# Performance work log

Hardware: AMD Instinct MI355X
Metric: run time of the kernel (lower is better)

The kernel has to match this reference:

```python
import jax, jax.numpy as jnp
import numpy as np

TOPK = 2


def _conv2d(x, w, b):
    # x: (B, Cin, H, W), w: (Cout, Cin, 3, 3), SAME padding (padding=1)
    y = jax.lax.conv_general_dilated(
        x, w, window_strides=(1, 1), padding='SAME',
        dimension_numbers=('NCHW', 'OIHW', 'NCHW'))
    return y + b[None, :, None, None]


def _msunit(x2d, c1w, c1b, c2w, c2b):
    # TimesNet-style 2D unit: conv(1->d_model) -> GELU -> conv(d_model->1)
    h = jax.nn.gelu(_conv2d(x2d, c1w, c1b))
    return _conv2d(h, c2w, c2b)


def setup_inputs():
    B, T, H, DM = 256, 2048, 720, 64
    key = jax.random.key(0)
    ks = jax.random.split(key, 5)
    x = jax.random.normal(ks[0], (B, 1, T), jnp.float32)
    conv1_w = jax.random.normal(ks[1], (DM, 1, 3, 3), jnp.float32) * 0.1
    conv1_b = jnp.zeros((DM,), jnp.float32)
    conv2_w = jax.random.normal(ks[2], (1, DM, 3, 3), jnp.float32) * 0.1
    conv2_b = jnp.zeros((1,), jnp.float32)
    head_w = jax.random.normal(ks[3], (H, T), jnp.float32) * 0.02
    head_b = jnp.zeros((H,), jnp.float32)
    return {'x': x, 'conv1_w': conv1_w, 'conv1_b': conv1_b,
            'conv2_w': conv2_w, 'conv2_b': conv2_b,
            'head_w': head_w, 'head_b': head_b}


def reference(x, conv1_w, conv1_b, conv2_w, conv2_b, head_w, head_b):
    B, _, T = x.shape
    # FFT amplitude spectrum, batch-averaged, drop DC bin
    amp = jnp.abs(jnp.fft.rfft(x[:, 0, :], axis=-1)).mean(0)[1:]
    vals, idx = jax.lax.top_k(amp, TOPK)
    # data-dependent period selection (mirrors .item() calls in torch -> Python ints)
    freqs = np.asarray(idx) + 1
    P_list = [max(1, int(round(T / int(f)))) for f in freqs]
    weights = jax.nn.softmax(vals.astype(x.dtype))
    y = jnp.zeros_like(x)
    for i, P in enumerate(P_list):
        cols = (T + P - 1) // P
        pad = P * cols - T
        xp = jnp.pad(x, ((0, 0), (0, 0), (0, pad)))
        x2d = xp.reshape(B, 1, cols, P).transpose(0, 1, 3, 2)  # (B,1,P,cols)
        y2d = _msunit(x2d, conv1_w, conv1_b, conv2_w, conv2_b)  # (B,1,P,cols)
        y1d = y2d.transpose(0, 1, 3, 2).reshape(B, 1, cols * P)[..., :T]
        y = y + weights[i] * y1d
    out = y[:, 0, :] @ head_w.T + head_b  # (B, horizon)
    return out
```

## Files before the change

### kernel.cpp

```cpp
#include <hip/hip_runtime.h>
#include <math.h>

#define T_LEN   2048
#define NB      256
#define N_FREQ  1024
#define DMODEL  64
#define HORIZON 720

#define WS_META 0
#define WS_AMP  64
#define WS_Y0   2048
#define WS_Y1   (2048 + NB * T_LEN)

#define PMAX_FAST 191
#define CHUNK   512
#define NCHUNK  4
#define HSTRIDE 904
#define ZSLOT   898
#define XSMAX   1312
#define ZXS     (XSMAX - 1)

typedef _Float16 h4 __attribute__((ext_vector_type(4)));
typedef float    fx4 __attribute__((ext_vector_type(4)));

__device__ __forceinline__ float gelu_fast(float a) {
    float a2 = a * a;
    float z  = a * fmaf(-0.07135481627159498f, a2, -1.5957691216057308f);
    float e  = __expf(z);
    return a * __builtin_amdgcn_rcpf(1.0f + e);
}

__device__ __forceinline__ float2 cmul(float2 a, float2 b) {
    return make_float2(a.x * b.x - a.y * b.y, a.x * b.y + a.y * b.x);
}

__device__ __forceinline__ unsigned magic_div(unsigned d) {
    return (unsigned)((0x100000000ULL + d - 1) / d);
}

__device__ __forceinline__ void compute_meta(const float* __restrict__ amp,
                                             float* sf, int* si, int tid,
                                             int& P1, int& cols1, int& P2, int& cols2,
                                             float& wg1, float& wg2) {
    float* v1s = sf;        float* v2s = sf + 256;
    int*   i1s = si;        int*   i2s = si + 256;
    float4 v4 = ((const float4*)amp)[tid];
    float vv[4] = {v4.x, v4.y, v4.z, v4.w};
    float v1 = -1e30f, v2 = -1e30f; int i1 = 1 << 30, i2 = 1 << 30;
    #pragma unroll
    for (int u = 0; u < 4; ++u) {
        int j = tid * 4 + u;
        float v = vv[u];
        if (v > v1) { v2 = v1; i2 = i1; v1 = v; i1 = j; }
        else if (v > v2) { v2 = v; i2 = j; }
    }
    v1s[tid] = v1; i1s[tid] = i1; v2s[tid] = v2; i2s[tid] = i2;
    __syncthreads();
    for (int st = 128; st > 0; st >>= 1) {
        if (tid < st) {
            float w1 = v1s[tid + st]; int j1 = i1s[tid + st];
            float w2 = v2s[tid + st]; int j2 = i2s[tid + st];
            float a1 = v1s[tid];      int a1i = i1s[tid];
            float a2 = v2s[tid];      int a2i = i2s[tid];
            float n1, n2; int n1i, n2i;
            bool w1_first = (w1 > a1) || (w1 == a1 && j1 < a1i);
            if (w1_first) {
                n1 = w1; n1i = j1;
                bool a1_next = (a1 > w2) || (a1 == w2 && a1i < j2);
                if (a1_next) { n2 = a1; n2i = a1i; } else { n2 = w2; n2i = j2; }
            } else {
                n1 = a1; n1i = a1i;
                bool w1_next = (w1 > a2) || (w1 == a2 && j1 < a2i);
                if (w1_next) { n2 = w1; n2i = j1; } else { n2 = a2; n2i = a2i; }
            }
            v1s[tid] = n1; i1s[tid] = n1i; v2s[tid] = n2; i2s[tid] = n2i;
        }
        __syncthreads();
    }
    float v1f = v1s[0], v2f = v2s[0];
    int f1 = i1s[0] + 1, f2 = i2s[0] + 1;
    __syncthreads();
    P1 = (int)llround(2048.0 / (double)f1); if (P1 < 1) P1 = 1;
    P2 = (int)llround(2048.0 / (double)f2); if (P2 < 1) P2 = 1;
    cols1 = (T_LEN + P1 - 1) / P1;
    cols2 = (T_LEN + P2 - 1) / P2;
    float mx = fmaxf(v1f, v2f);
    float e1 = __expf(v1f - mx), e2 = __expf(v2f - mx);
    float inv = 1.0f / (e1 + e2);
    wg1 = e1 * inv; wg2 = e2 * inv;
}

__global__ __launch_bounds__(256) void fft_amp_kernel(const float* __restrict__ x,
                                                      float* __restrict__ amp) {
    __shared__ float2 buf0[1024];
    __shared__ float2 buf1[1024];
    __shared__ float2 tw[512];
    const int tid = threadIdx.x;
    const int b = blockIdx.x;

    {
        float s, c;
        __sincosf((float)tid * 6.135923151542565e-3f, &s, &c);
        tw[tid] = make_float2(c, -s);
        __sincosf((float)(tid + 256) * 6.135923151542565e-3f, &s, &c);
        tw[tid + 256] = make_float2(c, -s);
    }
    const float2* xz = (const float2*)(x + b * T_LEN);
    buf0[tid]       = xz[tid];
    buf0[tid + 256] = xz[tid + 256];
    buf0[tid + 512] = xz[tid + 512];
    buf0[tid + 768] = xz[tid + 768];
    __syncthreads();

    float2* src = buf0;
    float2* dst = buf1;
    for (int s = 0; s < 10; s += 2) {
        const int Ns = 1 << s;
        const int j1 = tid;
        const int q  = j1 & (Ns - 1);
        const int hi = j1 >> s;
        float2 A = src[j1];
        float2 B = src[j1 + 512];
        float2 C = src[j1 + 256];
        float2 D = src[j1 + 768];
        float2 w  = tw[q << (9 - s)];
        float2 wB = cmul(w, B);
        float2 wD = cmul(w, D);
        float2 P0 = make_float2(A.x + wB.x, A.y + wB.y);
        float2 P1 = make_float2(A.x - wB.x, A.y - wB.y);
        float2 Q0 = make_float2(C.x + wD.x, C.y + wD.y);
        float2 Q1 = make_float2(C.x - wD.x, C.y - wD.y);
        float2 wa = tw[q << (8 - s)];
        float2 wb = tw[(q + Ns) << (8 - s)];
        float2 t0 = cmul(wa, Q0);
        float2 t1 = cmul(wb, Q1);
        const int O = (hi << (s + 2)) + q;
        dst[O]          = make_float2(P0.x + t0.x, P0.y + t0.y);
        dst[O + 2 * Ns] = make_float2(P0.x - t0.x, P0.y - t0.y);
        dst[O + Ns]     = make_float2(P1.x + t1.x, P1.y + t1.y);
        dst[O + 3 * Ns] = make_float2(P1.x - t1.x, P1.y - t1.y);
        __syncthreads();
        float2* tmp = src; src = dst; dst = tmp;
    }
    const int rot = (b * 8) & 1023;
    #pragma unroll
    for (int j = 0; j < 4; ++j) {
        const int kk = (tid + j * 256 + rot) & 1023;
        const int k  = kk + 1;
        float mag;
        if (k == 1024) {
            float2 Z0 = src[0];
            mag = fabsf(Z0.x - Z0.y) * (1.0f / 256.0f);
        } else {
            float2 Zk = src[k];
            float2 Zn = src[1024 - k];
            float Ax = 0.5f * (Zk.x + Zn.x), Ay = 0.5f * (Zk.y - Zn.y);
            float Bx = 0.5f * (Zk.y + Zn.y), By = -0.5f * (Zk.x - Zn.x);
            float sn, cs;
            __sincosf((float)k * 3.0679615757712823e-3f, &sn, &cs);
            float Xx = Ax + cs * Bx + sn * By;
            float Xy = Ay + cs * By - sn * Bx;
            mag = sqrtf(Xx * Xx + Xy * Xy) * (1.0f / 256.0f);
        }
        atomicAdd(amp + kk, mag);
    }
}

__global__ __launch_bounds__(256) void conv_fast_kernel(
    const float* __restrict__ x,
    const float* __restrict__ w1, const float* __restrict__ b1,
    const float* __restrict__ w2, const float* __restrict__ b2,
    const float* __restrict__ amp,
    float* __restrict__ ws, float* __restrict__ out)
{
    __shared__ float xs[XSMAX];
    __shared__ _Float16 dk[9][HSTRIDE];

    const int tid = threadIdx.x;
    {
        const int bid = blockIdx.y * gridDim.x + blockIdx.x;
        if (tid < 23) {
            int idx = bid * 23 + tid;
            if (idx < (NB * HORIZON) / 4)
                ((float4*)out)[idx] = make_float4(0.f, 0.f, 0.f, 0.f);
        }
    }

    int P1, cols1, P2, cols2; float wg1, wg2;
    compute_meta(amp, xs, (int*)(xs + 512), tid, P1, cols1, P2, cols2, wg1, wg2);

    if (blockIdx.x == 0 && blockIdx.y == 0 && tid == 0) {
        int* mi = (int*)ws;
        mi[0] = P1; mi[1] = cols1; mi[2] = P2; mi[3] = cols2;
        ws[4] = wg1; ws[5] = wg2;
    }

    const int per  = blockIdx.y;
    const int P    = per == 0 ? P1 : P2;
    const int cols = per == 0 ? cols1 : cols2;
    if (P > PMAX_FAST || P < 2) return;
    const float wgt = per == 0 ? wg1 : wg2;
    float* yout = ws + (per == 0 ? WS_Y0 : WS_Y1);

    const int b   = blockIdx.x >> 2;
    const int ci  = blockIdx.x & 3;
    const int t0  = ci * CHUNK;
    const int U0  = t0 - (P + 1);
    const int HN  = CHUNK + 2 * P + 2;
    const int X0  = t0 - (2 * P + 2);
    const int XN  = CHUNK + 4 * P + 4;
    const unsigned MP = magic_div((unsigned)P);

    __syncthreads();
    const int bT = b * T_LEN;
    for (int j = tid; j < XSMAX; j += 256) {
        int t = X0 + j;
        xs[j] = (j < XN && t >= 0 && t < T_LEN) ? x[bT + t] : 0.f;
    }
    __syncthreads();

    const int lane = tid & 63;
    const int wv   = tid >> 6;
    const int lm   = lane & 15;
    const int lg   = lane >> 4;

    h4  w1f[4], w2f[4];
    fx4 b1f[4];
    #pragma unroll
    for (int t = 0; t < 4; ++t) {
        #pragma unroll
        for (int i = 0; i < 4; ++i) {
            const int k = lg * 4 + i;
            w1f[t][i] = (_Float16)((k < 9) ? w1[(t * 16 + lm) * 9 + k] : 0.f);
            w2f[t][i] = (_Float16)((lm < 9) ? w2[(t * 16 + k) * 9 + lm] : 0.f);
            b1f[t][i] = b1[t * 16 + k];
        }
    }

    const int HN16 = (HN + 15) >> 4;
    const fx4 zf4 = {0.f, 0.f, 0.f, 0.f};

    for (int nt = wv; nt < HN16; nt += 4) {
        const int ih = nt * 16 + lm;
        const int u  = U0 + ih;
        const int uu = u < 0 ? 0 : u;
        const int cc = (int)__umulhi((unsigned)uu, MP);
        const int pp = uu - cc * P;
        const bool rm = pp > 0, rp = pp < P - 1, cm = cc > 0, cp = (cc + 1) < cols;
        const int ibase = ih + P + 1;
        h4 xb;
        #pragma unroll
        for (int j = 0; j < 4; ++j) {
            const int tap = lg * 4 + j;
            const int q = (tap * 86) >> 8;
            const int r = tap - q * 3;
            const bool ok = (tap < 9)
                && (q > 0 || rm) && (q < 2 || rp)
                && (r > 0 || cm) && (r < 2 || cp);
            const int addr = ok ? (ibase + (r - 1) * P + (q - 1)) : ZXS;
            xb[j] = (_Float16)xs[addr];
        }
        fx4 h0 = __builtin_amdgcn_mfma_f32_16x16x16f16(w1f[0], xb, b1f[0], 0, 0, 0);
        fx4 h1 = __builtin_amdgcn_mfma_f32_16x16x16f16(w1f[1], xb, b1f[1], 0, 0, 0);
        fx4 h2 = __builtin_amdgcn_mfma_f32_16x16x16f16(w1f[2], xb, b1f[2], 0, 0, 0);
        fx4 h3 = __builtin_amdgcn_mfma_f32_16x16x16f16(w1f[3], xb, b1f[3], 0, 0, 0);
        h4 g0, g1, g2, g3;
        #pragma unroll
        for (int i = 0; i < 4; ++i) {
            g0[i] = (_Float16)gelu_fast(h0[i]);
            g1[i] = (_Float16)gelu_fast(h1[i]);
            g2[i] = (_Float16)gelu_fast(h2[i]);
            g3[i] = (_Float16)gelu_fast(h3[i]);
        }
        fx4 da = __builtin_amdgcn_mfma_f32_16x16x16f16(w2f[0], g0, zf4, 0, 0, 0);
        fx4 db = __builtin_amdgcn_mfma_f32_16x16x16f16(w2f[1], g1, zf4, 0, 0, 0);
        da = __builtin_amdgcn_mfma_f32_16x16x16f16(w2f[2], g2, da, 0, 0, 0);
        db = __builtin_amdgcn_mfma_f32_16x16x16f16(w2f[3], g3, db, 0, 0, 0);
        if (ih < HN) {
            #pragma unroll
            for (int i = 0; i < 4; ++i) {
                const int row = lg * 4 + i;
                if (row < 9) dk[row][ih] = (_Float16)(da[i] + db[i]);
            }
        }
    }
    if (tid < 9) dk[tid][ZSLOT] = (_Float16)0.f;
    __syncthreads();

    const float bias2 = b2[0];
    #pragma unroll
    for (int o = 0; o < 2; ++o) {
        const int t = t0 + tid + o * 256;
        const int iout = tid + o * 256 + (P + 1);
        const int cc = (int)__umulhi((unsigned)t, MP);
        const int pp = t - cc * P;
        const bool rm = pp > 0, rp = pp < P - 1, cm = cc > 0, cp = (cc + 1) < cols;
        const int i0 = (rm && cm) ? iout - P - 1 : ZSLOT;
        const int i1 = rm         ? iout - 1     : ZSLOT;
        const int i2 = (rm && cp) ? iout + P - 1 : ZSLOT;
        const int i3 = cm         ? iout - P     : ZSLOT;
        const int i5 = cp         ? iout + P     : ZSLOT;
        const int i6 = (rp && cm) ? iout - P + 1 : ZSLOT;
        const int i7 = rp         ? iout + 1     : ZSLOT;
        const int i8 = (rp && cp) ? iout + P + 1 : ZSLOT;
        float s = (float)dk[4][iout];
        s += (float)dk[0][i0]; s += (float)dk[1][i1]; s += (float)dk[2][i2];
        s += (float)dk[3][i3]; s += (float)dk[5][i5]; s += (float)dk[6][i6];
        s += (float)dk[7][i7]; s += (float)dk[8][i8];
        yout[bT + t] = wgt * (s + bias2);
    }
}

__global__ __launch_bounds__(256) void conv_unit_kernel(
    const float* __restrict__ x,
    const float* __restrict__ w1, const float* __restrict__ b1,
    const float* __restrict__ w2, const float* __restrict__ b2,
    float* __restrict__ ws)
{
    const int* mi = (const int*)ws;
    const int per   = blockIdx.y;
    const int P     = mi[per * 2 + 0];
    const int cols  = mi[per * 2 + 1];
    if (P <= PMAX_FAST && P >= 2) return;
    const float wgt = ws[4 + per];
    float* yout = ws + (per == 0 ? WS_Y0 : WS_Y1);

    __shared__ float w1s[DMODEL * 9];
    __shared__ float w2s[DMODEL * 9];
    __shared__ float b1s[DMODEL];
    __shared__ float xs[12][13];
    __shared__ float hs[DMODEL][101];

    const int tid = threadIdx.x;
    for (int i = tid; i < DMODEL * 9; i += 256) { w1s[i] = w1[i]; w2s[i] = w2[i]; }
    if (tid < DMODEL) b1s[tid] = b1[tid];
    const float bias2 = b2[0];

    const int tp = (P + 7) >> 3;
    const int tc = (cols + 7) >> 3;
    const int tiles_img = tp * tc;
    const int total = tiles_img * NB;

    for (int tile = blockIdx.x; tile < total; tile += gridDim.x) {
        const int b   = tile / tiles_img;
        const int ti  = tile - b * tiles_img;
        const int tpi = ti / tc;
        const int tci = ti - tpi * tc;
        const int p0 = tpi * 8, c0 = tci * 8;

        __syncthreads();
        if (tid < 144) {
            int i = tid / 12, j = tid - (tid / 12) * 12;
            int pp = p0 - 2 + i, cc = c0 - 2 + j;
            float v = 0.f;
            if (pp >= 0 && pp < P && cc >= 0 && cc < cols) {
                int t = cc * P + pp;
                if (t < T_LEN) v = x[b * T_LEN + t];
            }
            xs[i][j] = v;
        }
        __syncthreads();

        #pragma unroll
        for (int it = 0; it < 25; ++it) {
            int idx = it * 256 + tid;
            int ch = idx / 100;
            int px = idx - ch * 100;
            int pi = px / 10;
            int pj = px - pi * 10;
            const float* w = &w1s[ch * 9];
            float a = b1s[ch];
            a = fmaf(w[0], xs[pi    ][pj    ], a);
            a = fmaf(w[1], xs[pi    ][pj + 1], a);
            a = fmaf(w[2], xs[pi    ][pj + 2], a);
            a = fmaf(w[3], xs[pi + 1][pj    ], a);
            a = fmaf(w[4], xs[pi + 1][pj + 1], a);
            a = fmaf(w[5], xs[pi + 1][pj + 2], a);
            a = fmaf(w[6], xs[pi + 2][pj    ], a);
            a = fmaf(w[7], xs[pi + 2][pj + 1], a);
            a = fmaf(w[8], xs[pi + 2][pj + 2], a);
            float g = gelu_fast(a);
            int pp = p0 - 1 + pi, cc = c0 - 1 + pj;
            bool in_img = (pp >= 0) & (pp < P) & (cc >= 0) & (cc < cols);
            hs[ch][px] = in_img ? g : 0.0f;
        }
        __syncthreads();

        {
            const int pixel = tid >> 2, part = tid & 3;
            const int pi = pixel >> 3, pj = pixel & 7;
            const int base = pi * 10 + pj;
            float s = 0.f;
            for (int ch = part * 16; ch < part * 16 + 16; ++ch) {
                const float* w  = &w2s[ch * 9];
                const float* hr = &hs[ch][base];
                s = fmaf(w[0], hr[0],  s);
                s = fmaf(w[1], hr[1],  s);
                s = fmaf(w[2], hr[2],  s);
                s = fmaf(w[3], hr[10], s);
                s = fmaf(w[4], hr[11], s);
                s = fmaf(w[5], hr[12], s);
                s = fmaf(w[6], hr[20], s);
                s = fmaf(w[7], hr[21], s);
                s = fmaf(w[8], hr[22], s);
            }
            s += __shfl_down(s, 1);
            s += __shfl_down(s, 2);
            if (part == 0) {
                int pp = p0 + pi, cc = c0 + pj;
                if (pp < P && cc < cols) {
                    int t = cc * P + pp;
                    if (t < T_LEN) yout[b * T_LEN + t] = wgt * (s + bias2);
                }
            }
        }
    }
}

__global__ __launch_bounds__(256) void head_gemm_kernel(
    const float* __restrict__ ws, const float* __restrict__ hw,
    const float* __restrict__ hb, float* __restrict__ out)
{
    const float* y0 = ws + WS_Y0;
    const float* y1 = ws + WS_Y1;
    const int b0 = blockIdx.x * 32, h0 = blockIdx.y * 32;
    const int kc0 = blockIdx.z * 512;
    __shared__ float As[32][33];
    __shared__ float Bs[32][33];
    const int tid = threadIdx.x;
    const int tx = tid & 15, ty = tid >> 4;
    const int i0 = ty * 2, j0 = tx * 2;
    const int sr = tid >> 3;
    const int sc = (tid & 7) * 4;
    float a00 = 0.f, a01 = 0.f, a10 = 0.f, a11 = 0.f;
    for (int k0 = kc0; k0 < kc0 + 512; k0 += 32) {
        {
            const int src = (b0 + sr) * T_LEN + k0 + sc;
            float4 u = *(const float4*)(y0 + src);
            float4 v = *(const float4*)(y1 + src);
            As[sr][sc]     = u.x + v.x;
            As[sr][sc + 1] = u.y + v.y;
            As[sr][sc + 2] = u.z + v.z;
            As[sr][sc + 3] = u.w + v.w;
            const int hrow = h0 + sr;
            float4 w = (hrow < HORIZON) ? *(const float4*)(hw + hrow * T_LEN + k0 + sc)
                                        : make_float4(0.f, 0.f, 0.f, 0.f);
            Bs[sr][sc]     = w.x;
            Bs[sr][sc + 1] = w.y;
            Bs[sr][sc + 2] = w.z;
            Bs[sr][sc + 3] = w.w;
        }
        __syncthreads();
        #pragma unroll
        for (int kk = 0; kk < 32; ++kk) {
            float av0 = As[i0][kk], av1 = As[i0 + 1][kk];
            float bv0 = Bs[j0][kk], bv1 = Bs[j0 + 1][kk];
            a00 = fmaf(av0, bv0, a00); a01 = fmaf(av0, bv1, a01);
            a10 = fmaf(av1, bv0, a10); a11 = fmaf(av1, bv1, a11);
        }
        __syncthreads();
    }
    const int bi = b0 + i0, hj = h0 + j0;
    if (blockIdx.z == 0) {
        if (hj < HORIZON)     { float bb = hb[hj];     a00 += bb; a10 += bb; }
        if (hj + 1 < HORIZON) { float bb = hb[hj + 1]; a01 += bb; a11 += bb; }
    }
    if (hj < HORIZON) {
        atomicAdd(&out[bi * HORIZON + hj], a00);
        atomicAdd(&out[(bi + 1) * HORIZON + hj], a10);
    }
    if (hj + 1 < HORIZON) {
        atomicAdd(&out[bi * HORIZON + hj + 1], a01);
        atomicAdd(&out[(bi + 1) * HORIZON + hj + 1], a11);
    }
}

extern "C" void kernel_launch(void* const* d_in, const int* in_sizes, int n_in,
                              void* d_out, int out_size, void* d_ws, size_t ws_size,
                              hipStream_t stream) {
    const float* x   = (const float*)d_in[0];
    const float* c1w = (const float*)d_in[1];
    const float* c1b = (const float*)d_in[2];
    const float* c2w = (const float*)d_in[3];
    const float* c2b = (const float*)d_in[4];
    const float* hw  = (const float*)d_in[5];
    const float* hb  = (const float*)d_in[6];
    float* out = (float*)d_out;
    float* ws  = (float*)d_ws;

    float* amp = ws + WS_AMP;

    hipMemsetAsync(amp, 0, N_FREQ * sizeof(float), stream);
    fft_amp_kernel<<<NB, 256, 0, stream>>>(x, amp);
    conv_fast_kernel<<<dim3(NB * NCHUNK, 2), 256, 0, stream>>>(x, c1w, c1b, c2w, c2b, amp, ws, out);
    conv_unit_kernel<<<dim3(256, 2), 256, 0, stream>>>(x, c1w, c1b, c2w, c2b, ws);
    head_gemm_kernel<<<dim3(NB / 32, (HORIZON + 31) / 32, 4), 256, 0, stream>>>(ws, hw, hb, out);
}
```

Baseline: 157.5 us.

## Merge conv fast and fallback kernels, enlarge conv chunks, retile head GEMM to 4x4

The fast MFMA conv path and the generic fallback are merged into one kernel that branches on period, using a shared raw shared-memory buffer. This removes a kernel launch and the metadata round-trip through workspace. Conv chunks double to 1024 samples, halving the block count and the halo overhead per sample. The head GEMM moves to 64x64 tiles with 4x4 register blocking, transposed shared-memory tiles and a split-K of 256. The price is more shared memory per block and more atomic partial sums in the GEMM.

```diff
diff --git a/kernel.cpp b/kernel.cpp
--- a/kernel.cpp
+++ b/kernel.cpp
@@ -7,17 +7,16 @@
 #define DMODEL  64
 #define HORIZON 720
 
-#define WS_META 0
 #define WS_AMP  64
 #define WS_Y0   2048
 #define WS_Y1   (2048 + NB * T_LEN)
 
 #define PMAX_FAST 191
-#define CHUNK   512
-#define NCHUNK  4
-#define HSTRIDE 904
-#define ZSLOT   898
-#define XSMAX   1312
+#define CHUNK   1024
+#define NCHUNK  2
+#define HSTRIDE 1412
+#define ZSLOT   1408
+#define XSMAX   1824
 #define ZXS     (XSMAX - 1)
 
 typedef _Float16 h4 __attribute__((ext_vector_type(4)));
@@ -166,21 +165,22 @@
     }
 }
 
-__global__ __launch_bounds__(256) void conv_fast_kernel(
+__global__ __launch_bounds__(256) void conv_all_kernel(
     const float* __restrict__ x,
     const float* __restrict__ w1, const float* __restrict__ b1,
     const float* __restrict__ w2, const float* __restrict__ b2,
     const float* __restrict__ amp,
     float* __restrict__ ws, float* __restrict__ out)
 {
-    __shared__ float xs[XSMAX];
-    __shared__ _Float16 dk[9][HSTRIDE];
+    __shared__ __align__(16) char smem_raw[32720];
+    float* xs = (float*)smem_raw;
+    _Float16 (*dk)[HSTRIDE] = (_Float16 (*)[HSTRIDE])(smem_raw + XSMAX * 4);
 
     const int tid = threadIdx.x;
     {
         const int bid = blockIdx.y * gridDim.x + blockIdx.x;
-        if (tid < 23) {
-            int idx = bid * 23 + tid;
+        if (tid < 45) {
+            int idx = bid * 45 + tid;
             if (idx < (NB * HORIZON) / 4)
                 ((float4*)out)[idx] = make_float4(0.f, 0.f, 0.f, 0.f);
         }
@@ -188,290 +188,290 @@
 
     int P1, cols1, P2, cols2; float wg1, wg2;
     compute_meta(amp, xs, (int*)(xs + 512), tid, P1, cols1, P2, cols2, wg1, wg2);
-
-    if (blockIdx.x == 0 && blockIdx.y == 0 && tid == 0) {
-        int* mi = (int*)ws;
-        mi[0] = P1; mi[1] = cols1; mi[2] = P2; mi[3] = cols2;
-        ws[4] = wg1; ws[5] = wg2;
-    }
 
     const int per  = blockIdx.y;
     const int P    = per == 0 ? P1 : P2;
     const int cols = per == 0 ? cols1 : cols2;
-    if (P > PMAX_FAST || P < 2) return;
     const float wgt = per == 0 ? wg1 : wg2;
     float* yout = ws + (per == 0 ? WS_Y0 : WS_Y1);
 
-    const int b   = blockIdx.x >> 2;
-    const int ci  = blockIdx.x & 3;
-    const int t0  = ci * CHUNK;
-    const int U0  = t0 - (P + 1);
-    const int HN  = CHUNK + 2 * P + 2;
-    const int X0  = t0 - (2 * P + 2);
-    const int XN  = CHUNK + 4 * P + 4;
-    const unsigned MP = magic_div((unsigned)P);
-
-    __syncthreads();
-    const int bT = b * T_LEN;
-    for (int j = tid; j < XSMAX; j += 256) {
-        int t = X0 + j;
-        xs[j] = (j < XN && t >= 0 && t < T_LEN) ? x[bT + t] : 0.f;
-    }
-    __syncthreads();
-
-    const int lane = tid & 63;
-    const int wv   = tid >> 6;
-    const int lm   = lane & 15;
-    const int lg   = lane >> 4;
-
-    h4  w1f[4], w2f[4];
-    fx4 b1f[4];
-    #pragma unroll
-    for (int t = 0; t < 4; ++t) {
+    if (P >= 2 && P <= PMAX_FAST) {
+        const int b   = blockIdx.x >> 1;
+        const int ci  = blockIdx.x & 1;
+        const int t0  = ci * CHUNK;
+        const int U0  = t0 - (P + 1);
+        const int HN  = CHUNK + 2 * P + 2;
+        const int X0  = t0 - (2 * P + 2);
+        const int XN  = CHUNK + 4 * P + 4;
+        const unsigned MP = magic_div((unsigned)P);
+
+        __syncthreads();
+        const int bT = b * T_LEN;
+        for (int j = tid; j < XSMAX; j += 256) {
+            int t = X0 + j;
+            xs[j] = (j < XN && t >= 0 && t < T_LEN) ? x[bT + t] : 0.f;
+        }
+        __syncthreads();
+
+        const int lane = tid & 63;
+        const int wv   = tid >> 6;
+        const int lm   = lane & 15;
+        const int lg   = lane >> 4;
+
+        h4  w1f[4], w2f[4];
+        fx4 b1f[4];
         #pragma unroll
-        for (int i = 0; i < 4; ++i) {
-            const int k = lg * 4 + i;
-            w1f[t][i] = (_Float16)((k < 9) ? w1[(t * 16 + lm) * 9 + k] : 0.f);
-            w2f[t][i] = (_Float16)((lm < 9) ? w2[(t * 16 + k) * 9 + lm] : 0.f);
-            b1f[t][i] = b1[t * 16 + k];
-        }
-    }
-
-    const int HN16 = (HN + 15) >> 4;
-    const fx4 zf4 = {0.f, 0.f, 0.f, 0.f};
-
-    for (int nt = wv; nt < HN16; nt += 4) {
-        const int ih = nt * 16 + lm;
-        const int u  = U0 + ih;
-        const int uu = u < 0 ? 0 : u;
-        const int cc = (int)__umulhi((unsigned)uu, MP);
-        const int pp = uu - cc * P;
-        const bool rm = pp > 0, rp = pp < P - 1, cm = cc > 0, cp = (cc + 1) < cols;
-        const int ibase = ih + P + 1;
-        h4 xb;
-        #pragma unroll
-        for (int j = 0; j < 4; ++j) {
-            const int tap = lg * 4 + j;
-            const int q = (tap * 86) >> 8;
-            const int r = tap - q * 3;
-            const bool ok = (tap < 9)
-                && (q > 0 || rm) && (q < 2 || rp)
-                && (r > 0 || cm) && (r < 2 || cp);
-            const int addr = ok ? (ibase + (r - 1) * P + (q - 1)) : ZXS;
-            xb[j] = (_Float16)xs[addr];
-        }
-        fx4 h0 = __builtin_amdgcn_mfma_f32_16x16x16f16(w1f[0], xb, b1f[0], 0, 0, 0);
-        fx4 h1 = __builtin_amdgcn_mfma_f32_16x16x16f16(w1f[1], xb, b1f[1], 0, 0, 0);
-        fx4 h2 = __builtin_amdgcn_mfma_f32_16x16x16f16(w1f[2], xb, b1f[2], 0, 0, 0);
-        fx4 h3 = __builtin_amdgcn_mfma_f32_16x16x16f16(w1f[3], xb, b1f[3], 0, 0, 0);
-        h4 g0, g1, g2, g3;
-        #pragma unroll
-        for (int i = 0; i < 4; ++i) {
-            g0[i] = (_Float16)gelu_fast(h0[i]);
-            g1[i] = (_Float16)gelu_fast(h1[i]);
-            g2[i] = (_Float16)gelu_fast(h2[i]);
-            g3[i] = (_Float16)gelu_fast(h3[i]);
-        }
-        fx4 da = __builtin_amdgcn_mfma_f32_16x16x16f16(w2f[0], g0, zf4, 0, 0, 0);
-        fx4 db = __builtin_amdgcn_mfma_f32_16x16x16f16(w2f[1], g1, zf4, 0, 0, 0);
-        da = __builtin_amdgcn_mfma_f32_16x16x16f16(w2f[2], g2, da, 0, 0, 0);
-        db = __builtin_amdgcn_mfma_f32_16x16x16f16(w2f[3], g3, db, 0, 0, 0);
-        if (ih < HN) {
+        for (int t = 0; t < 4; ++t) {
             #pragma unroll
             for (int i = 0; i < 4; ++i) {
-                const int row = lg * 4 + i;
-                if (row < 9) dk[row][ih] = (_Float16)(da[i] + db[i]);
-            }
-        }
-    }
-    if (tid < 9) dk[tid][ZSLOT] = (_Float16)0.f;
-    __syncthreads();
-
-    const float bias2 = b2[0];
-    #pragma unroll
-    for (int o = 0; o < 2; ++o) {
-        const int t = t0 + tid + o * 256;
-        const int iout = tid + o * 256 + (P + 1);
-        const int cc = (int)__umulhi((unsigned)t, MP);
-        const int pp = t - cc * P;
-        const bool rm = pp > 0, rp = pp < P - 1, cm = cc > 0, cp = (cc + 1) < cols;
-        const int i0 = (rm && cm) ? iout - P - 1 : ZSLOT;
-        const int i1 = rm         ? iout - 1     : ZSLOT;
-        const int i2 = (rm && cp) ? iout + P - 1 : ZSLOT;
-        const int i3 = cm         ? iout - P     : ZSLOT;
-        const int i5 = cp         ? iout + P     : ZSLOT;
-        const int i6 = (rp && cm) ? iout - P + 1 : ZSLOT;
-        const int i7 = rp         ? iout + 1     : ZSLOT;
-        const int i8 = (rp && cp) ? iout + P + 1 : ZSLOT;
-        float s = (float)dk[4][iout];
-        s += (float)dk[0][i0]; s += (float)dk[1][i1]; s += (float)dk[2][i2];
-        s += (float)dk[3][i3]; s += (float)dk[5][i5]; s += (float)dk[6][i6];
-        s += (float)dk[7][i7]; s += (float)dk[8][i8];
-        yout[bT + t] = wgt * (s + bias2);
-    }
-}
-
-__global__ __launch_bounds__(256) void conv_unit_kernel(
-    const float* __restrict__ x,
-    const float* __restrict__ w1, const float* __restrict__ b1,
-    const float* __restrict__ w2, const float* __restrict__ b2,
-    float* __restrict__ ws)
-{
-    const int* mi = (const int*)ws;
-    const int per   = blockIdx.y;
-    const int P     = mi[per * 2 + 0];
-    const int cols  = mi[per * 2 + 1];
-    if (P <= PMAX_FAST && P >= 2) return;
-    const float wgt = ws[4 + per];
-    float* yout = ws + (per == 0 ? WS_Y0 : WS_Y1);
-
-    __shared__ float w1s[DMODEL * 9];
-    __shared__ float w2s[DMODEL * 9];
-    __shared__ float b1s[DMODEL];
-    __shared__ float xs[12][13];
-    __shared__ float hs[DMODEL][101];
-
-    const int tid = threadIdx.x;
-    for (int i = tid; i < DMODEL * 9; i += 256) { w1s[i] = w1[i]; w2s[i] = w2[i]; }
-    if (tid < DMODEL) b1s[tid] = b1[tid];
-    const float bias2 = b2[0];
-
-    const int tp = (P + 7) >> 3;
-    const int tc = (cols + 7) >> 3;
-    const int tiles_img = tp * tc;
-    const int total = tiles_img * NB;
-
-    for (int tile = blockIdx.x; tile < total; tile += gridDim.x) {
-        const int b   = tile / tiles_img;
-        const int ti  = tile - b * tiles_img;
-        const int tpi = ti / tc;
-        const int tci = ti - tpi * tc;
-        const int p0 = tpi * 8, c0 = tci * 8;
-
-        __syncthreads();
-        if (tid < 144) {
-            int i = tid / 12, j = tid - (tid / 12) * 12;
-            int pp = p0 - 2 + i, cc = c0 - 2 + j;
-            float v = 0.f;
-            if (pp >= 0 && pp < P && cc >= 0 && cc < cols) {
-                int t = cc * P + pp;
-                if (t < T_LEN) v = x[b * T_LEN + t];
-            }
-            xs[i][j] = v;
-        }
-        __syncthreads();
-
+                const int k = lg * 4 + i;
+                w1f[t][i] = (_Float16)((k < 9) ? w1[(t * 16 + lm) * 9 + k] : 0.f);
+                w2f[t][i] = (_Float16)((lm < 9) ? w2[(t * 16 + k) * 9 + lm] : 0.f);
+                b1f[t][i] = b1[t * 16 + k];
+            }
+        }
+
+        const int HN16 = (HN + 15) >> 4;
+        const fx4 zf4 = {0.f, 0.f, 0.f, 0.f};
+
+        for (int nt = wv; nt < HN16; nt += 4) {
+            const int ih = nt * 16 + lm;
+            const int u  = U0 + ih;
+            const int uu = u < 0 ? 0 : u;
+            const int cc = (int)__umulhi((unsigned)uu, MP);
+            const int pp = uu - cc * P;
+            const bool rm = pp > 0, rp = pp < P - 1, cm = cc > 0, cp = (cc + 1) < cols;
+            const int ibase = ih + P + 1;
+            h4 xb;
+            #pragma unroll
+            for (int j = 0; j < 4; ++j) {
+                const int tap = lg * 4 + j;
+                const int q = (tap * 86) >> 8;
+                const int r = tap - q * 3;
+                const bool ok = (tap < 9)
+                    && (q > 0 || rm) && (q < 2 || rp)
+                    && (r > 0 || cm) && (r < 2 || cp);
+                const int addr = ok ? (ibase + (r - 1) * P + (q - 1)) : ZXS;
+                xb[j] = (_Float16)xs[addr];
+            }
+            fx4 h0 = __builtin_amdgcn_mfma_f32_16x16x16f16(w1f[0], xb, b1f[0], 0, 0, 0);
+            fx4 h1 = __builtin_amdgcn_mfma_f32_16x16x16f16(w1f[1], xb, b1f[1], 0, 0, 0);
+            fx4 h2 = __builtin_amdgcn_mfma_f32_16x16x16f16(w1f[2], xb, b1f[2], 0, 0, 0);
+            fx4 h3 = __builtin_amdgcn_mfma_f32_16x16x16f16(w1f[3], xb, b1f[3], 0, 0, 0);
+            h4 g0, g1, g2, g3;
+            #pragma unroll
+            for (int i = 0; i < 4; ++i) {
+                g0[i] = (_Float16)gelu_fast(h0[i]);
+                g1[i] = (_Float16)gelu_fast(h1[i]);
+                g2[i] = (_Float16)gelu_fast(h2[i]);
+                g3[i] = (_Float16)gelu_fast(h3[i]);
+            }
+            fx4 da = __builtin_amdgcn_mfma_f32_16x16x16f16(w2f[0], g0, zf4, 0, 0, 0);
+            fx4 db = __builtin_amdgcn_mfma_f32_16x16x16f16(w2f[1], g1, zf4, 0, 0, 0);
+            da = __builtin_amdgcn_mfma_f32_16x16x16f16(w2f[2], g2, da, 0, 0, 0);
+            db = __builtin_amdgcn_mfma_f32_16x16x16f16(w2f[3], g3, db, 0, 0, 0);
+            if (ih < HN) {
+                #pragma unroll
+                for (int i = 0; i < 4; ++i) {
+                    const int row = lg * 4 + i;
+                    if (row < 9) dk[row][ih] = (_Float16)(da[i] + db[i]);
+                }
+            }
+        }
+        if (tid < 9) dk[tid][ZSLOT] = (_Float16)0.f;
+        __syncthreads();
+
+        const float bias2 = b2[0];
         #pragma unroll
-        for (int it = 0; it < 25; ++it) {
-            int idx = it * 256 + tid;
-            int ch = idx / 100;
-            int px = idx - ch * 100;
-            int pi = px / 10;
-            int pj = px - pi * 10;
-            const float* w = &w1s[ch * 9];
-            float a = b1s[ch];
-            a = fmaf(w[0], xs[pi    ][pj    ], a);
-            a = fmaf(w[1], xs[pi    ][pj + 1], a);
-            a = fmaf(w[2], xs[pi    ][pj + 2], a);
-            a = fmaf(w[3], xs[pi + 1][pj    ], a);
-            a = fmaf(w[4], xs[pi + 1][pj + 1], a);
-            a = fmaf(w[5], xs[pi + 1][pj + 2], a);
-            a = fmaf(w[6], xs[pi + 2][pj    ], a);
-            a = fmaf(w[7], xs[pi + 2][pj + 1], a);
-            a = fmaf(w[8], xs[pi + 2][pj + 2], a);
-            float g = gelu_fast(a);
-            int pp = p0 - 1 + pi, cc = c0 - 1 + pj;
-            bool in_img = (pp >= 0) & (pp < P) & (cc >= 0) & (cc < cols);
-            hs[ch][px] = in_img ? g : 0.0f;
-        }
-        __syncthreads();
-
-        {
-            const int pixel = tid >> 2, part = tid & 3;
-            const int pi = pixel >> 3, pj = pixel & 7;
-            const int base = pi * 10 + pj;
-            float s = 0.f;
-            for (int ch = part * 16; ch < part * 16 + 16; ++ch) {
-                const float* w  = &w2s[ch * 9];
-                const float* hr = &hs[ch][base];
-                s = fmaf(w[0], hr[0],  s);
-                s = fmaf(w[1], hr[1],  s);
-                s = fmaf(w[2], hr[2],  s);
-                s = fmaf(w[3], hr[10], s);
-                s = fmaf(w[4], hr[11], s);
-                s = fmaf(w[5], hr[12], s);
-                s = fmaf(w[6], hr[20], s);
-                s = fmaf(w[7], hr[21], s);
-                s = fmaf(w[8], hr[22], s);
-            }
-            s += __shfl_down(s, 1);
-            s += __shfl_down(s, 2);
-            if (part == 0) {
-                int pp = p0 + pi, cc = c0 + pj;
-                if (pp < P && cc < cols) {
+        for (int o = 0; o < 4; ++o) {
+            const int t = t0 + tid + o * 256;
+            const int iout = tid + o * 256 + (P + 1);
+            const int cc = (int)__umulhi((unsigned)t, MP);
+            const int pp = t - cc * P;
+            const bool rm = pp > 0, rp = pp < P - 1, cm = cc > 0, cp = (cc + 1) < cols;
+            const int i0 = (rm && cm) ? iout - P - 1 : ZSLOT;
+            const int i1 = rm         ? iout - 1     : ZSLOT;
+            const int i2 = (rm && cp) ? iout + P - 1 : ZSLOT;
+            const int i3 = cm         ? iout - P     : ZSLOT;
+            const int i5 = cp         ? iout + P     : ZSLOT;
+            const int i6 = (rp && cm) ? iout - P + 1 : ZSLOT;
+            const int i7 = rp         ? iout + 1     : ZSLOT;
+            const int i8 = (rp && cp) ? iout + P + 1 : ZSLOT;
+            float s = (float)dk[4][iout];
+            s += (float)dk[0][i0]; s += (float)dk[1][i1]; s += (float)dk[2][i2];
+            s += (float)dk[3][i3]; s += (float)dk[5][i5]; s += (float)dk[6][i6];
+            s += (float)dk[7][i7]; s += (float)dk[8][i8];
+            yout[bT + t] = wgt * (s + bias2);
+        }
+    } else {
+        float* w1s = (float*)smem_raw;
+        float* w2s = w1s + 576;
+        float* b1s = w2s + 576;
+        float (*fxs)[13] = (float (*)[13])(b1s + 64);
+        float (*hs)[101]  = (float (*)[101])(b1s + 64 + 156);
+
+        for (int i = tid; i < DMODEL * 9; i += 256) { w1s[i] = w1[i]; w2s[i] = w2[i]; }
+        if (tid < DMODEL) b1s[tid] = b1[tid];
+        const float bias2 = b2[0];
+
+        const int tp = (P + 7) >> 3;
+        const int tc = (cols + 7) >> 3;
+        const int tiles_img = tp * tc;
+        const int total = tiles_img * NB;
+
+        for (int tile = blockIdx.x; tile < total; tile += gridDim.x) {
+            const int b   = tile / tiles_img;
+            const int ti  = tile - b * tiles_img;
+            const int tpi = ti / tc;
+            const int tci = ti - tpi * tc;
+            const int p0 = tpi * 8, c0 = tci * 8;
+
+            __syncthreads();
+            if (tid < 144) {
+                int i = tid / 12, j = tid - (tid / 12) * 12;
+                int pp = p0 - 2 + i, cc = c0 - 2 + j;
+                float v = 0.f;
+                if (pp >= 0 && pp < P && cc >= 0 && cc < cols) {
                     int t = cc * P + pp;
-                    if (t < T_LEN) yout[b * T_LEN + t] = wgt * (s + bias2);
+                    if (t < T_LEN) v = x[b * T_LEN + t];
                 }
-            }
-        }
-    }
-}
-
+                fxs[i][j] = v;
+            }
+            __syncthreads();
+
+            #pragma unroll
+            for (int it = 0; it < 25; ++it) {
+                int idx = it * 256 + tid;
+                int ch = idx / 100;
+                int px = idx - ch * 100;
+                int pi = px / 10;
+                int pj = px - pi * 10;
+                const float* w = &w1s[ch * 9];
+                float a = b1s[ch];
+                a = fmaf(w[0], fxs[pi    ][pj    ], a);
+                a = fmaf(w[1], fxs[pi    ][pj + 1], a);
+                a = fmaf(w[2], fxs[pi    ][pj + 2], a);
+                a = fmaf(w[3], fxs[pi + 1][pj    ], a);
+                a = fmaf(w[4], fxs[pi + 1][pj + 1], a);
+                a = fmaf(w[5], fxs[pi + 1][pj + 2], a);
+                a = fmaf(w[6], fxs[pi + 2][pj    ], a);
+                a = fmaf(w[7], fxs[pi + 2][pj + 1], a);
+                a = fmaf(w[8], fxs[pi + 2][pj + 2], a);
+                float g = gelu_fast(a);
+                int pp = p0 - 1 + pi, cc = c0 - 1 + pj;
+                bool in_img = (pp >= 0) & (pp < P) & (cc >= 0) & (cc < cols);
+                hs[ch][px] = in_img ? g : 0.0f;
+            }
+            __syncthreads();
+
+            {
+                const int pixel = tid >> 2, part = tid & 3;
+                const int pi = pixel >> 3, pj = pixel & 7;
+                const int base = pi * 10 + pj;
+                float s = 0.f;
+                for (int ch = part * 16; ch < part * 16 + 16; ++ch) {
+                    const float* w  = &w2s[ch * 9];
+                    const float* hr = &hs[ch][base];
+                    s = fmaf(w[0], hr[0],  s);
+                    s = fmaf(w[1], hr[1],  s);
+                    s = fmaf(w[2], hr[2],  s);
+                    s = fmaf(w[3], hr[10], s);
+                    s = fmaf(w[4], hr[11], s);
+                    s = fmaf(w[5], hr[12], s);
+                    s = fmaf(w[6], hr[20], s);
+                    s = fmaf(w[7], hr[21], s);
+                    s = fmaf(w[8], hr[22], s);
+                }
+                s += __shfl_down(s, 1);
+                s += __shfl_down(s, 2);
+                if (part == 0) {
+                    int pp = p0 + pi, cc = c0 + pj;
+                    if (pp < P && cc < cols) {
+                        int t = cc * P + pp;
+                        if (t < T_LEN) yout[b * T_LEN + t] = wgt * (s + bias2);
+                    }
+                }
+            }
+        }
+    }
+}
+
+#define HG_KC 256
 __global__ __launch_bounds__(256) void head_gemm_kernel(
     const float* __restrict__ ws, const float* __restrict__ hw,
     const float* __restrict__ hb, float* __restrict__ out)
 {
     const float* y0 = ws + WS_Y0;
     const float* y1 = ws + WS_Y1;
-    const int b0 = blockIdx.x * 32, h0 = blockIdx.y * 32;
-    const int kc0 = blockIdx.z * 512;
-    __shared__ float As[32][33];
-    __shared__ float Bs[32][33];
+    const int b0 = blockIdx.x * 64, h0 = blockIdx.y * 64;
+    const int kc0 = blockIdx.z * HG_KC;
+    __shared__ float As[32][68];
+    __shared__ float Bs[32][68];
     const int tid = threadIdx.x;
-    const int tx = tid & 15, ty = tid >> 4;
-    const int i0 = ty * 2, j0 = tx * 2;
-    const int sr = tid >> 3;
-    const int sc = (tid & 7) * 4;
-    float a00 = 0.f, a01 = 0.f, a10 = 0.f, a11 = 0.f;
-    for (int k0 = kc0; k0 < kc0 + 512; k0 += 32) {
+    const int i0 = (tid & 15) * 4;
+    const int j0 = (tid >> 4) * 4;
+    const int r0 = tid >> 3,        q0 = (tid & 7) * 4;
+    const int r1 = (tid + 256) >> 3, q1 = q0;
+    float acc[4][4] = {{0.f}};
+    for (int k0 = kc0; k0 < kc0 + HG_KC; k0 += 32) {
         {
-            const int src = (b0 + sr) * T_LEN + k0 + sc;
-            float4 u = *(const float4*)(y0 + src);
-            float4 v = *(const float4*)(y1 + src);
-            As[sr][sc]     = u.x + v.x;
-            As[sr][sc + 1] = u.y + v.y;
-            As[sr][sc + 2] = u.z + v.z;
-            As[sr][sc + 3] = u.w + v.w;
-            const int hrow = h0 + sr;
-            float4 w = (hrow < HORIZON) ? *(const float4*)(hw + hrow * T_LEN + k0 + sc)
-                                        : make_float4(0.f, 0.f, 0.f, 0.f);
-            Bs[sr][sc]     = w.x;
-            Bs[sr][sc + 1] = w.y;
-            Bs[sr][sc + 2] = w.z;
-            Bs[sr][sc + 3] = w.w;
+            const int s0 = (b0 + r0) * T_LEN + k0 + q0;
+            float4 u = *(const float4*)(y0 + s0);
+            float4 v = *(const float4*)(y1 + s0);
+            As[q0 + 0][r0] = u.x + v.x; As[q0 + 1][r0] = u.y + v.y;
+            As[q0 + 2][r0] = u.z + v.z; As[q0 + 3][r0] = u.w + v.w;
+            const int s1 = (b0 + r1) * T_LEN + k0 + q1;
+            u = *(const float4*)(y0 + s1);
+            v = *(const float4*)(y1 + s1);
+            As[q1 + 0][r1] = u.x + v.x; As[q1 + 1][r1] = u.y + v.y;
+            As[q1 + 2][r1] = u.z + v.z; As[q1 + 3][r1] = u.w + v.w;
+            const int hr0 = h0 + r0;
+            float4 w = (hr0 < HORIZON) ? *(const float4*)(hw + hr0 * T_LEN + k0 + q0)
+                                       : make_float4(0.f, 0.f, 0.f, 0.f);
+            Bs[q0 + 0][r0] = w.x; Bs[q0 + 1][r0] = w.y;
+            Bs[q0 + 2][r0] = w.z; Bs[q0 + 3][r0] = w.w;
+            const int hr1 = h0 + r1;
+            w = (hr1 < HORIZON) ? *(const float4*)(hw + hr1 * T_LEN + k0 + q1)
+                                : make_float4(0.f, 0.f, 0.f, 0.f);
+            Bs[q1 + 0][r1] = w.x; Bs[q1 + 1][r1] = w.y;
+            Bs[q1 + 2][r1] = w.z; Bs[q1 + 3][r1] = w.w;
         }
         __syncthreads();
         #pragma unroll
         for (int kk = 0; kk < 32; ++kk) {
-            float av0 = As[i0][kk], av1 = As[i0 + 1][kk];
-            float bv0 = Bs[j0][kk], bv1 = Bs[j0 + 1][kk];
-            a00 = fmaf(av0, bv0, a00); a01 = fmaf(av0, bv1, a01);
-            a10 = fmaf(av1, bv0, a10); a11 = fmaf(av1, bv1, a11);
-        }
-        __syncthreads();
-    }
-    const int bi = b0 + i0, hj = h0 + j0;
-    if (blockIdx.z == 0) {
-        if (hj < HORIZON)     { float bb = hb[hj];     a00 += bb; a10 += bb; }
-        if (hj + 1 < HORIZON) { float bb = hb[hj + 1]; a01 += bb; a11 += bb; }
-    }
-    if (hj < HORIZON) {
-        atomicAdd(&out[bi * HORIZON + hj], a00);
-        atomicAdd(&out[(bi + 1) * HORIZON + hj], a10);
-    }
-    if (hj + 1 < HORIZON) {
-        atomicAdd(&out[bi * HORIZON + hj + 1], a01);
-        atomicAdd(&out[(bi + 1) * HORIZON + hj + 1], a11);
+            float4 av = *(const float4*)&As[kk][i0];
+            float4 bv = *(const float4*)&Bs[kk][j0];
+            acc[0][0] = fmaf(av.x, bv.x, acc[0][0]);
+            acc[0][1] = fmaf(av.x, bv.y, acc[0][1]);
+            acc[0][2] = fmaf(av.x, bv.z, acc[0][2]);
+            acc[0][3] = fmaf(av.x, bv.w, acc[0][3]);
+            acc[1][0] = fmaf(av.y, bv.x, acc[1][0]);
+            acc[1][1] = fmaf(av.y, bv.y, acc[1][1]);
+            acc[1][2] = fmaf(av.y, bv.z, acc[1][2]);
+            acc[1][3] = fmaf(av.y, bv.w, acc[1][3]);
+            acc[2][0] = fmaf(av.z, bv.x, acc[2][0]);
+            acc[2][1] = fmaf(av.z, bv.y, acc[2][1]);
+            acc[2][2] = fmaf(av.z, bv.z, acc[2][2]);
+            acc[2][3] = fmaf(av.z, bv.w, acc[2][3]);
+            acc[3][0] = fmaf(av.w, bv.x, acc[3][0]);
+            acc[3][1] = fmaf(av.w, bv.y, acc[3][1]);
+            acc[3][2] = fmaf(av.w, bv.z, acc[3][2]);
+            acc[3][3] = fmaf(av.w, bv.w, acc[3][3]);
+        }
+        __syncthreads();
+    }
+    #pragma unroll
+    for (int i = 0; i < 4; ++i) {
+        const int bi = b0 + i0 + i;
+        #pragma unroll
+        for (int j = 0; j < 4; ++j) {
+            const int hj = h0 + j0 + j;
+            if (hj < HORIZON) {
+                float v = acc[i][j];
+                if (blockIdx.z == 0) v += hb[hj];
+                atomicAdd(&out[bi * HORIZON + hj], v);
+            }
+        }
     }
 }
 
@@ -492,7 +492,6 @@
 
     hipMemsetAsync(amp, 0, N_FREQ * sizeof(float), stream);
     fft_amp_kernel<<<NB, 256, 0, stream>>>(x, amp);
-    conv_fast_kernel<<<dim3(NB * NCHUNK, 2), 256, 0, stream>>>(x, c1w, c1b, c2w, c2b, amp, ws, out);
-    conv_unit_kernel<<<dim3(256, 2), 256, 0, stream>>>(x, c1w, c1b, c2w, c2b, ws);
-    head_gemm_kernel<<<dim3(NB / 32, (HORIZON + 31) / 32, 4), 256, 0, stream>>>(ws, hw, hb, out);
-}
+    conv_all_kernel<<<dim3(NB * NCHUNK, 2), 256, 0, stream>>>(x, c1w, c1b, c2w, c2b, amp, ws, out);
+    head_gemm_kernel<<<dim3(NB / 64, (HORIZON + 63) / 64, T_LEN / HG_KC), 256, 0, stream>>>(ws, hw, hb, out);
+}
```

Result: slower. 195.9 us (+24.4%).

## Use fp16 MFMA for head GEMM without split-K; double conv chunk size

Applied to the files above, without the earlier changes.

The head GEMM is rewritten to use 16x16x16 fp16 MFMA instructions over the full K range per block. This removes the split-K atomics, so the zeroing of the output inside the conv kernel is dropped and results are stored directly. The conv fast kernel also processes 1024-sample chunks instead of 512, which halves the redundant halo work at the cost of more shared memory and fewer blocks. Rounding the activations and head weights to fp16 reduces precision, and with 184 output tiles each reducing a K of 2048 the GEMM grid is small.

```diff
diff --git a/kernel.cpp b/kernel.cpp
--- a/kernel.cpp
+++ b/kernel.cpp
@@ -7,17 +7,16 @@
 #define DMODEL  64
 #define HORIZON 720
 
-#define WS_META 0
 #define WS_AMP  64
 #define WS_Y0   2048
 #define WS_Y1   (2048 + NB * T_LEN)
 
 #define PMAX_FAST 191
-#define CHUNK   512
-#define NCHUNK  4
-#define HSTRIDE 904
-#define ZSLOT   898
-#define XSMAX   1312
+#define CHUNK   1024
+#define NCHUNK  2
+#define HSTRIDE 1412
+#define ZSLOT   1408
+#define XSMAX   1824
 #define ZXS     (XSMAX - 1)
 
 typedef _Float16 h4 __attribute__((ext_vector_type(4)));
@@ -177,14 +176,6 @@
     __shared__ _Float16 dk[9][HSTRIDE];
 
     const int tid = threadIdx.x;
-    {
-        const int bid = blockIdx.y * gridDim.x + blockIdx.x;
-        if (tid < 23) {
-            int idx = bid * 23 + tid;
-            if (idx < (NB * HORIZON) / 4)
-                ((float4*)out)[idx] = make_float4(0.f, 0.f, 0.f, 0.f);
-        }
-    }
 
     int P1, cols1, P2, cols2; float wg1, wg2;
     compute_meta(amp, xs, (int*)(xs + 512), tid, P1, cols1, P2, cols2, wg1, wg2);
@@ -202,8 +193,8 @@
     const float wgt = per == 0 ? wg1 : wg2;
     float* yout = ws + (per == 0 ? WS_Y0 : WS_Y1);
 
-    const int b   = blockIdx.x >> 2;
-    const int ci  = blockIdx.x & 3;
+    const int b   = blockIdx.x >> 1;
+    const int ci  = blockIdx.x & 1;
     const int t0  = ci * CHUNK;
     const int U0  = t0 - (P + 1);
     const int HN  = CHUNK + 2 * P + 2;
@@ -289,7 +280,7 @@
 
     const float bias2 = b2[0];
     #pragma unroll
-    for (int o = 0; o < 2; ++o) {
+    for (int o = 0; o < 4; ++o) {
         const int t = t0 + tid + o * 256;
         const int iout = tid + o * 256 + (P + 1);
         const int cc = (int)__umulhi((unsigned)t, MP);
@@ -417,61 +408,64 @@
     }
 }
 
+#define HG_KC 64
 __global__ __launch_bounds__(256) void head_gemm_kernel(
     const float* __restrict__ ws, const float* __restrict__ hw,
     const float* __restrict__ hb, float* __restrict__ out)
 {
+    __shared__ _Float16 As[32][72];
+    __shared__ _Float16 Bs[32][72];
     const float* y0 = ws + WS_Y0;
     const float* y1 = ws + WS_Y1;
+    const int tid = threadIdx.x;
     const int b0 = blockIdx.x * 32, h0 = blockIdx.y * 32;
-    const int kc0 = blockIdx.z * 512;
-    __shared__ float As[32][33];
-    __shared__ float Bs[32][33];
-    const int tid = threadIdx.x;
-    const int tx = tid & 15, ty = tid >> 4;
-    const int i0 = ty * 2, j0 = tx * 2;
-    const int sr = tid >> 3;
-    const int sc = (tid & 7) * 4;
-    float a00 = 0.f, a01 = 0.f, a10 = 0.f, a11 = 0.f;
-    for (int k0 = kc0; k0 < kc0 + 512; k0 += 32) {
-        {
-            const int src = (b0 + sr) * T_LEN + k0 + sc;
+    const int lane = tid & 63;
+    const int wv   = tid >> 6;
+    const int lm   = lane & 15;
+    const int lg   = lane >> 4;
+    const int wm   = (wv & 1) * 16;
+    const int wn   = (wv >> 1) * 16;
+    const int sr = tid >> 4;
+    const int sq = (tid & 15) * 4;
+
+    fx4 acc = {0.f, 0.f, 0.f, 0.f};
+
+    for (int k0 = 0; k0 < T_LEN; k0 += HG_KC) {
+        #pragma unroll
+        for (int hh = 0; hh < 2; ++hh) {
+            const int r = sr + hh * 16;
+            const int src = (b0 + r) * T_LEN + k0 + sq;
             float4 u = *(const float4*)(y0 + src);
             float4 v = *(const float4*)(y1 + src);
-            As[sr][sc]     = u.x + v.x;
-            As[sr][sc + 1] = u.y + v.y;
-            As[sr][sc + 2] = u.z + v.z;
-            As[sr][sc + 3] = u.w + v.w;
-            const int hrow = h0 + sr;
-            float4 w = (hrow < HORIZON) ? *(const float4*)(hw + hrow * T_LEN + k0 + sc)
-                                        : make_float4(0.f, 0.f, 0.f, 0.f);
-            Bs[sr][sc]     = w.x;
-            Bs[sr][sc + 1] = w.y;
-            Bs[sr][sc + 2] = w.z;
-            Bs[sr][sc + 3] = w.w;
-        }
-        __syncthreads();
-        #pragma unroll
-        for (int kk = 0; kk < 32; ++kk) {
-            float av0 = As[i0][kk], av1 = As[i0 + 1][kk];
-            float bv0 = Bs[j0][kk], bv1 = Bs[j0 + 1][kk];
-            a00 = fmaf(av0, bv0, a00); a01 = fmaf(av0, bv1, a01);
-            a10 = fmaf(av1, bv0, a10); a11 = fmaf(av1, bv1, a11);
-        }
-        __syncthreads();
-    }
-    const int bi = b0 + i0, hj = h0 + j0;
-    if (blockIdx.z == 0) {
-        if (hj < HORIZON)     { float bb = hb[hj];     a00 += bb; a10 += bb; }
-        if (hj + 1 < HORIZON) { float bb = hb[hj + 1]; a01 += bb; a11 += bb; }
-    }
-    if (hj < HORIZON) {
-        atomicAdd(&out[bi * HORIZON + hj], a00);
-        atomicAdd(&out[(bi + 1) * HORIZON + hj], a10);
-    }
-    if (hj + 1 < HORIZON) {
-        atomicAdd(&out[bi * HORIZON + hj + 1], a01);
-        atomicAdd(&out[(bi + 1) * HORIZON + hj + 1], a11);
+            As[r][sq + 0] = (_Float16)(u.x + v.x);
+            As[r][sq + 1] = (_Float16)(u.y + v.y);
+            As[r][sq + 2] = (_Float16)(u.z + v.z);
+            As[r][sq + 3] = (_Float16)(u.w + v.w);
+            const int hr = h0 + r;
+            float4 w = (hr < HORIZON) ? *(const float4*)(hw + hr * T_LEN + k0 + sq)
+                                      : make_float4(0.f, 0.f, 0.f, 0.f);
+            Bs[r][sq + 0] = (_Float16)w.x;
+            Bs[r][sq + 1] = (_Float16)w.y;
+            Bs[r][sq + 2] = (_Float16)w.z;
+            Bs[r][sq + 3] = (_Float16)w.w;
+        }
+        __syncthreads();
+        #pragma unroll
+        for (int kk = 0; kk < HG_KC; kk += 16) {
+            h4 af = *(const h4*)&As[wm + lm][kk + lg * 4];
+            h4 bf = *(const h4*)&Bs[wn + lm][kk + lg * 4];
+            acc = __builtin_amdgcn_mfma_f32_16x16x16f16(af, bf, acc, 0, 0, 0);
+        }
+        __syncthreads();
+    }
+    const int ncol = h0 + wn + lm;
+    if (ncol < HORIZON) {
+        const float bb = hb[ncol];
+        #pragma unroll
+        for (int i = 0; i < 4; ++i) {
+            const int m = b0 + wm + lg * 4 + i;
+            out[m * HORIZON + ncol] = acc[i] + bb;
+        }
     }
 }
 
@@ -494,5 +488,5 @@
     fft_amp_kernel<<<NB, 256, 0, stream>>>(x, amp);
     conv_fast_kernel<<<dim3(NB * NCHUNK, 2), 256, 0, stream>>>(x, c1w, c1b, c2w, c2b, amp, ws, out);
     conv_unit_kernel<<<dim3(256, 2), 256, 0, stream>>>(x, c1w, c1b, c2w, c2b, ws);
-    head_gemm_kernel<<<dim3(NB / 32, (HORIZON + 31) / 32, 4), 256, 0, stream>>>(ws, hw, hb, out);
-}
+    head_gemm_kernel<<<dim3(NB / 32, (HORIZON + 31) / 32), 256, 0, stream>>>(ws, hw, hb, out);
+}
```

New measurement: 165.9 us. 5.3% more time.
